# Performance work log

Measured on AMD Instinct MI355X. Metric: run time of the kernel, lower is better.

Reference implementation:

```python
import jax, jax.numpy as jnp
import numpy as np

K_HOP = 2

def _graph_conv(x, A, W, b):
    feats = [x]
    xk = x
    for _ in range(K_HOP):
        xk = jnp.einsum('bmn,bnc->bmc', A, xk)
        feats.append(xk)
    return jnp.concatenate(feats, -1) @ W + b

def _pair_mlp(y, W2, b2, W1, b1, shape):
    # normal_conv: fc1(relu(fc2(y))).reshape(shape)
    return (jax.nn.relu(y @ W2 + b2) @ W1 + b1).reshape(shape)

def setup_inputs():
    key = jax.random.key(0)
    ks = jax.random.split(key, 16)
    B, T, N = 8, 12, 200
    C_IN, H, D, H_ST = 2, 64, 32, 64
    def lin(k, fi, fo):
        k1, k2 = jax.random.split(k)
        s = 1.0 / float(np.sqrt(fi))
        return (jax.random.uniform(k1, (fi, fo), jnp.float32, -s, s),
                jax.random.uniform(k2, (fo,), jnp.float32, -s, s))
    W_s2d, b_s2d = lin(ks[0], H_ST, D)
    W_rz, b_rz = lin(ks[1], 1 + D, 2 * D)
    W_h, b_h = lin(ks[2], 1 + D, D)
    Wc2, bc2 = lin(ks[3], 2 * D, D)
    Wc1, bc1 = lin(ks[4], D, 1)
    Wm2, bm2 = lin(ks[5], 2 * D, D)
    Wm1, bm1 = lin(ks[6], D, 1)
    gin = (C_IN + H) * (1 + K_HOP)
    W_ru, b_ru = lin(ks[7], gin, 2 * H)
    W_cand, b_cand = lin(ks[8], gin, H)
    Wp1, bp1 = lin(ks[9], H, H)
    Wp2, bp2 = lin(ks[10], H, 1)
    x = jax.random.normal(ks[11], (B, T, N, C_IN), jnp.float32)
    node_fea_st = jax.random.normal(ks[12], (N, H_ST), jnp.float32)
    return dict(x=x, node_fea_st=node_fea_st, W_s2d=W_s2d, b_s2d=b_s2d,
                W_rz=W_rz, b_rz=b_rz, W_h=W_h, b_h=b_h,
                Wc2=Wc2, bc2=bc2, Wc1=Wc1, bc1=bc1,
                Wm2=Wm2, bm2=bm2, Wm1=Wm1, bm1=bm1,
                W_ru=W_ru, b_ru=b_ru, W_cand=W_cand, b_cand=b_cand,
                Wp1=Wp1, bp1=bp1, Wp2=Wp2, bp2=bp2)

def reference(x, node_fea_st, W_s2d, b_s2d, W_rz, b_rz, W_h, b_h,
              Wc2, bc2, Wc1, bc1, Wm2, bm2, Wm1, bm1,
              W_ru, b_ru, W_cand, b_cand, Wp1, bp1, Wp2, bp2):
    B, T, N, _ = x.shape
    H = W_cand.shape[1]
    D = W_h.shape[1]
    # states_dy init: linear_s2d(node_fea_st) broadcast over batch
    state_dy0 = jnp.broadcast_to((node_fea_st @ W_s2d + b_s2d)[None], (B, N, D))
    state0 = jnp.zeros((B, N, H), x.dtype)
    xs = jnp.transpose(x, (1, 0, 2, 3))  # [T,B,N,C]

    def step(carry, xt):
        state, state_dy = carry
        inp1 = xt[..., :1]
        # DynamicGraphGRU (conv_method='normal')
        rz = jax.nn.sigmoid(jnp.concatenate([inp1, state_dy], -1) @ W_rz + b_rz)
        r, z = jnp.split(rz, 2, -1)
        h = jnp.tanh(jnp.concatenate([inp1, r * state_dy], -1) @ W_h + b_h)
        new_dy = z * state_dy + (1.0 - z) * h
        s = jax.nn.relu(new_dy)  # [B,N,D]
        y = jnp.concatenate([jnp.broadcast_to(s[:, :, None, :], (B, N, N, D)),
                             jnp.broadcast_to(s[:, None, :, :], (B, N, N, D))], -1)
        g = _pair_mlp(y, Wc2, bc2, Wc1, bc1, (B, N, N))
        m = _pair_mlp(y, Wm2, bm2, Wm1, bm1, (B, N, N))
        A = g * jax.nn.sigmoid(m)  # dynamic graph [B,N,N]
        # DCGRUCell with supports=[A]
        ru = jax.nn.sigmoid(_graph_conv(jnp.concatenate([xt, state], -1), A, W_ru, b_ru))
        rr, u = jnp.split(ru, 2, -1)
        c = jnp.tanh(_graph_conv(jnp.concatenate([xt, rr * state], -1), A, W_cand, b_cand))
        new_state = u * state + (1.0 - u) * c
        return (new_state, new_dy), A

    (state, _), dy_graphs = jax.lax.scan(step, (state0, state_dy0), xs)
    # predictor: Linear -> LeakyReLU -> Linear
    pred = jax.nn.leaky_relu(state @ Wp1 + bp1) @ Wp2 + bp2  # [B,N,1]
    return pred, dy_graphs
```

## Files before the change

kernel.cpp:

```cpp
#include <hip/hip_runtime.h>
#include <math.h>

#define B_ 8
#define T_ 12
#define N_ 200
#define R_ 1600
#define NN_ 40000

__device__ __forceinline__ float sigm(float v) { return 1.f / (1.f + expf(-v)); }

__global__ void __launch_bounds__(256) k_dyall(
        const float* __restrict__ x,  const float* __restrict__ nf,
        const float* __restrict__ Ws2d, const float* __restrict__ bs2d,
        const float* __restrict__ Wrz,  const float* __restrict__ brz,
        const float* __restrict__ Wh,   const float* __restrict__ bh,
        const float* __restrict__ Wc2,  const float* __restrict__ Wm2,
        const float* __restrict__ bc2,  const float* __restrict__ bm2,
        float* __restrict__ Pc, float* __restrict__ Qc,
        float* __restrict__ Pm, float* __restrict__ Qm,
        float* __restrict__ state) {
    __shared__ alignas(16) float sWs2d[64 * 32];
    __shared__ alignas(16) float sWrzT[64][36];
    __shared__ alignas(16) float sWhT[32][36];
    __shared__ alignas(16) float sWc2T[32][68];
    __shared__ alignas(16) float sWm2T[32][68];
    __shared__ float sbrz[64], sbh[32], sbs2d[32], sbc2[32], sbm2[32];
    __shared__ alignas(16) float nfs[4][64], dy[4][32], rz[4][64], s4[4][32];
    __shared__ alignas(16) float in1[4][36], in2[4][36];
    int bk = blockIdx.x, tid = threadIdx.x;
    int w = tid >> 6, o = tid & 63;
    int row = bk * 4 + w, b = row / N_, n = row % N_;
    state[bk * 256 + tid] = 0.f;
    for (int idx = tid; idx < 2048; idx += 256) sWs2d[idx] = Ws2d[idx];
    for (int idx = tid; idx < 2304; idx += 256) {
        int oo = idx / 36, ii = idx % 36;
        sWrzT[oo][ii] = (ii < 33) ? Wrz[ii * 64 + oo] : 0.f;
    }
    for (int idx = tid; idx < 1152; idx += 256) {
        int kk = idx / 36, ii = idx % 36;
        sWhT[kk][ii] = (ii < 33) ? Wh[ii * 32 + kk] : 0.f;
    }
    for (int idx = tid; idx < 2176; idx += 256) {
        int kk = idx / 68, rr = idx % 68;
        float vc = (rr < 64) ? Wc2[rr * 32 + kk] : 0.f;
        float vm = (rr < 64) ? Wm2[rr * 32 + kk] : 0.f;
        sWc2T[kk][rr] = vc; sWm2T[kk][rr] = vm;
    }
    if (tid < 144) { ((float*)in1)[tid] = 0.f; ((float*)in2)[tid] = 0.f; }
    if (tid < 64) sbrz[tid] = brz[tid];
    if (tid < 32) { sbh[tid] = bh[tid]; sbs2d[tid] = bs2d[tid];
                    sbc2[tid] = bc2[tid]; sbm2[tid] = bm2[tid]; }
    nfs[w][o] = nf[n * 64 + o];
    __syncthreads();
    if (o < 32) {
        float acc = sbs2d[o];
        #pragma unroll 8
        for (int i = 0; i < 64; ++i) acc += nfs[w][i] * sWs2d[i * 32 + o];
        dy[w][o] = acc;
    }
    __syncthreads();
    for (int t = 0; t < T_; ++t) {
        if (o == 0) { float v = x[((b * T_ + t) * N_ + n) * 2]; in1[w][0] = v; in2[w][0] = v; }
        if (o < 32) in1[w][o + 1] = dy[w][o];
        __syncthreads();
        float acc = sbrz[o];
        #pragma unroll
        for (int ig = 0; ig < 9; ++ig) {
            float4 w4 = *(const float4*)&sWrzT[o][4 * ig];
            float4 f4 = *(const float4*)&in1[w][4 * ig];
            acc += f4.x * w4.x + f4.y * w4.y + f4.z * w4.z + f4.w * w4.w;
        }
        rz[w][o] = sigm(acc);
        __syncthreads();
        if (o < 32) in2[w][o + 1] = rz[w][o] * dy[w][o];
        __syncthreads();
        if (o < 32) {
            float h = sbh[o];
            #pragma unroll
            for (int ig = 0; ig < 9; ++ig) {
                float4 w4 = *(const float4*)&sWhT[o][4 * ig];
                float4 f4 = *(const float4*)&in2[w][4 * ig];
                h += f4.x * w4.x + f4.y * w4.y + f4.z * w4.z + f4.w * w4.w;
            }
            h = tanhf(h);
            float z = rz[w][32 + o];
            float nd = z * dy[w][o] + (1.f - z) * h;
            dy[w][o] = nd;
            s4[w][o] = nd > 0.f ? nd : 0.f;
        }
        __syncthreads();
        size_t base = ((size_t)t * R_ + row) * 32;
        for (int idx = o; idx < 128; idx += 64) {
            int mat = idx >> 5, k = idx & 31;
            const float* WT = (mat < 2) ? &sWc2T[k][0] : &sWm2T[k][0];
            int rb = (mat & 1) ? 32 : 0;
            float a = (mat == 0) ? sbc2[k] : (mat == 2) ? sbm2[k] : 0.f;
            #pragma unroll
            for (int ig = 0; ig < 8; ++ig) {
                float4 w4 = *(const float4*)&WT[rb + 4 * ig];
                float4 f4 = *(const float4*)&s4[w][4 * ig];
                a += f4.x * w4.x + f4.y * w4.y + f4.z * w4.z + f4.w * w4.w;
            }
            ((mat == 0) ? Pc : (mat == 1) ? Qc : (mat == 2) ? Pm : Qm)[base + k] = a;
        }
        __syncthreads();
    }
}

__global__ void __launch_bounds__(256) k_pairall(
        const float* __restrict__ Pc, const float* __restrict__ Qc,
        const float* __restrict__ Pm, const float* __restrict__ Qm,
        const float* __restrict__ Wc1, const float* __restrict__ bc1,
        const float* __restrict__ Wm1, const float* __restrict__ bm1,
        float* __restrict__ out) {
    __shared__ float sPc[16][36], sQc[16][36], sPm[16][36], sQm[16][36];
    int z = blockIdx.z;
    int i0 = blockIdx.x * 16, j0 = blockIdx.y * 16;
    int tid = threadIdx.y * 16 + threadIdx.x;
    size_t tb = (size_t)z * N_;
    for (int l = tid; l < 128; l += 256) {
        int r = l >> 3, q = l & 7;
        int gi = i0 + r, gj = j0 + r;
        float4 z4 = make_float4(0.f, 0.f, 0.f, 0.f);
        *(float4*)&sPc[r][4 * q] = (gi < N_) ? *(const float4*)&Pc[(tb + gi) * 32 + 4 * q] : z4;
        *(float4*)&sPm[r][4 * q] = (gi < N_) ? *(const float4*)&Pm[(tb + gi) * 32 + 4 * q] : z4;
        *(float4*)&sQc[r][4 * q] = (gj < N_) ? *(const float4*)&Qc[(tb + gj) * 32 + 4 * q] : z4;
        *(float4*)&sQm[r][4 * q] = (gj < N_) ? *(const float4*)&Qm[(tb + gj) * 32 + 4 * q] : z4;
    }
    float4 wc[8], wm[8];
    #pragma unroll
    for (int kg = 0; kg < 8; ++kg) {
        wc[kg] = *(const float4*)&Wc1[4 * kg];
        wm[kg] = *(const float4*)&Wm1[4 * kg];
    }
    __syncthreads();
    int i = i0 + threadIdx.y, j = j0 + threadIdx.x;
    if (i >= N_ || j >= N_) return;
    int ty = threadIdx.y, tx = threadIdx.x;
    float g0 = 0.f, g1 = 0.f, m0 = 0.f, m1 = 0.f;
    #pragma unroll
    for (int kg = 0; kg < 8; ++kg) {
        float4 pc = *(const float4*)&sPc[ty][4 * kg];
        float4 qc = *(const float4*)&sQc[tx][4 * kg];
        float4 w4 = wc[kg];
        g0 += fmaxf(pc.x + qc.x, 0.f) * w4.x + fmaxf(pc.y + qc.y, 0.f) * w4.y;
        g1 += fmaxf(pc.z + qc.z, 0.f) * w4.z + fmaxf(pc.w + qc.w, 0.f) * w4.w;
        float4 pm = *(const float4*)&sPm[ty][4 * kg];
        float4 qm = *(const float4*)&sQm[tx][4 * kg];
        float4 v4 = wm[kg];
        m0 += fmaxf(pm.x + qm.x, 0.f) * v4.x + fmaxf(pm.y + qm.y, 0.f) * v4.y;
        m1 += fmaxf(pm.z + qm.z, 0.f) * v4.z + fmaxf(pm.w + qm.w, 0.f) * v4.w;
    }
    float g = g0 + g1 + bc1[0];
    float m = m0 + m1 + bm1[0];
    out[R_ + (((size_t)z * N_ + i) * N_ + j)] = g * sigm(m);
}

__global__ void __launch_bounds__(256) k_a2(
        const float* __restrict__ Abase, float* __restrict__ Cbase, int nmat) {
    __shared__ float Ast[32][132];
    __shared__ float Bs[32][68];
    int bx = blockIdx.x;
    int z = bx % nmat, tl = bx / nmat;
    int i0 = (tl >> 2) * 128, j0 = (tl & 3) * 64;
    const float* Az = Abase + (size_t)z * NN_;
    float* Cz = Cbase + (size_t)z * NN_;
    int tid = threadIdx.x;
    int tx = tid & 15, ty = tid >> 4;
    float acc[8][4] = {};
    for (int k0 = 0; k0 < 200; k0 += 32) {
        {
            int i = tid >> 1;
            int kb = (tid & 1) * 16;
            int gi = i0 + i;
            #pragma unroll
            for (int q = 0; q < 4; ++q) {
                int k = kb + q * 4;
                int gk = k0 + k;
                float4 v = make_float4(0.f, 0.f, 0.f, 0.f);
                if (gi < N_) {
                    if (gk + 3 < N_) v = *(const float4*)&Az[gi * N_ + gk];
                    else {
                        float t0 = (gk + 0 < N_) ? Az[gi * N_ + gk + 0] : 0.f;
                        float t1 = (gk + 1 < N_) ? Az[gi * N_ + gk + 1] : 0.f;
                        float t2 = (gk + 2 < N_) ? Az[gi * N_ + gk + 2] : 0.f;
                        float t3 = (gk + 3 < N_) ? Az[gi * N_ + gk + 3] : 0.f;
                        v = make_float4(t0, t1, t2, t3);
                    }
                }
                Ast[k + 0][i] = v.x; Ast[k + 1][i] = v.y;
                Ast[k + 2][i] = v.z; Ast[k + 3][i] = v.w;
            }
        }
        {
            #pragma unroll
            for (int q = 0; q < 2; ++q) {
                int id = tid + 256 * q;
                int k = id >> 4, jq = (id & 15) * 4;
                int gk = k0 + k, gj = j0 + jq;
                float4 v = make_float4(0.f, 0.f, 0.f, 0.f);
                if (gk < N_) {
                    if (gj + 3 < N_) v = *(const float4*)&Az[gk * N_ + gj];
                    else {
                        float t0 = (gj + 0 < N_) ? Az[gk * N_ + gj + 0] : 0.f;
                        float t1 = (gj + 1 < N_) ? Az[gk * N_ + gj + 1] : 0.f;
                        float t2 = (gj + 2 < N_) ? Az[gk * N_ + gj + 2] : 0.f;
                        float t3 = (gj + 3 < N_) ? Az[gk * N_ + gj + 3] : 0.f;
                        v = make_float4(t0, t1, t2, t3);
                    }
                }
                *(float4*)&Bs[k][jq] = v;
            }
        }
        __syncthreads();
        #pragma unroll 8
        for (int k = 0; k < 32; ++k) {
            float4 a0 = *(const float4*)&Ast[k][ty * 8];
            float4 a1 = *(const float4*)&Ast[k][ty * 8 + 4];
            float4 bv = *(const float4*)&Bs[k][tx * 4];
            acc[0][0] += a0.x * bv.x; acc[0][1] += a0.x * bv.y; acc[0][2] += a0.x * bv.z; acc[0][3] += a0.x * bv.w;
            acc[1][0] += a0.y * bv.x; acc[1][1] += a0.y * bv.y; acc[1][2] += a0.y * bv.z; acc[1][3] += a0.y * bv.w;
            acc[2][0] += a0.z * bv.x; acc[2][1] += a0.z * bv.y; acc[2][2] += a0.z * bv.z; acc[2][3] += a0.z * bv.w;
            acc[3][0] += a0.w * bv.x; acc[3][1] += a0.w * bv.y; acc[3][2] += a0.w * bv.z; acc[3][3] += a0.w * bv.w;
            acc[4][0] += a1.x * bv.x; acc[4][1] += a1.x * bv.y; acc[4][2] += a1.x * bv.z; acc[4][3] += a1.x * bv.w;
            acc[5][0] += a1.y * bv.x; acc[5][1] += a1.y * bv.y; acc[5][2] += a1.y * bv.z; acc[5][3] += a1.y * bv.w;
            acc[6][0] += a1.z * bv.x; acc[6][1] += a1.z * bv.y; acc[6][2] += a1.z * bv.z; acc[6][3] += a1.z * bv.w;
            acc[7][0] += a1.w * bv.x; acc[7][1] += a1.w * bv.y; acc[7][2] += a1.w * bv.z; acc[7][3] += a1.w * bv.w;
        }
        __syncthreads();
    }
    #pragma unroll
    for (int r = 0; r < 8; ++r) {
        int gi = i0 + ty * 8 + r;
        if (gi >= N_) continue;
        int gj = j0 + tx * 4;
        if (gj + 3 < N_) {
            *(float4*)&Cz[gi * N_ + gj] = make_float4(acc[r][0], acc[r][1], acc[r][2], acc[r][3]);
        } else {
            #pragma unroll
            for (int e = 0; e < 4; ++e) if (gj + e < N_) Cz[gi * N_ + gj + e] = acc[r][e];
        }
    }
}

__global__ void __launch_bounds__(256) k_xh(
        const float* __restrict__ Abase, const float* __restrict__ A2base,
        const float* __restrict__ x, int z0, float* __restrict__ xh) {
    __shared__ float xtl[400];
    int zl = blockIdx.x, tid = threadIdx.x;
    int z = z0 + zl, t = z >> 3, b = z & 7;
    int w = tid >> 6, l = tid & 63;
    const float* xb = x + ((size_t)(b * T_ + t)) * N_ * 2;
    for (int idx = tid; idx < 400; idx += 256) xtl[idx] = xb[idx];
    __syncthreads();
    for (int it = 0; it < 50; ++it) {
        int i = it * 4 + w;
        float p0 = 0.f, p1 = 0.f, p2 = 0.f, p3 = 0.f;
        if (l < 50) {
            float4 a4 = *(const float4*)(Abase + (size_t)zl * NN_ + i * 200 + 4 * l);
            float4 c4 = *(const float4*)(A2base + (size_t)zl * NN_ + i * 200 + 4 * l);
            #pragma unroll
            for (int q = 0; q < 4; ++q) {
                float av = (&a4.x)[q], cv = (&c4.x)[q];
                float x0 = xtl[(4 * l + q) * 2], x1 = xtl[(4 * l + q) * 2 + 1];
                p0 += av * x0; p1 += av * x1; p2 += cv * x0; p3 += cv * x1;
            }
        }
        #pragma unroll
        for (int off = 32; off > 0; off >>= 1) {
            p0 += __shfl_down(p0, off); p1 += __shfl_down(p1, off);
            p2 += __shfl_down(p2, off); p3 += __shfl_down(p3, off);
        }
        if (l == 0) *(float4*)(xh + ((size_t)zl * N_ + i) * 4) = make_float4(p0, p1, p2, p3);
    }
}

__global__ void __launch_bounds__(256) k_ru2(
        const float* __restrict__ At, const float* __restrict__ A2t,
        const float* __restrict__ xht,
        const float* __restrict__ x, int t, const float* __restrict__ state,
        const float* __restrict__ Wru, const float* __restrict__ bru,
        float* __restrict__ rs, float* __restrict__ ub) {
    __shared__ float a2s[2 * 200], c2s[2 * 200];
    __shared__ float hpA[4][64], hpC[4][64];
    __shared__ float feat[2][200];
    __shared__ float gp[8][2][128];
    int bx = blockIdx.x;
    int b = bx & 7, i0 = (bx >> 3) * 2;
    int tid = threadIdx.x;
    const float* F = state + (size_t)b * (N_ * 64);
    {
        const float4* Ar = (const float4*)(At + ((size_t)b * N_ + i0) * 200);
        const float4* Cr = (const float4*)(A2t + ((size_t)b * N_ + i0) * 200);
        if (tid < 100) { ((float4*)a2s)[tid] = Ar[tid]; ((float4*)c2s)[tid] = Cr[tid]; }
        if (tid >= 100 && tid < 164) {
            int l = tid - 100, r = l >> 5, q = l & 31;
            *(float2*)&feat[r][2 + 2 * q] = *(const float2*)&F[(size_t)(i0 + r) * 64 + 2 * q];
        }
        if (tid >= 164 && tid < 168) {
            int l = tid - 164;
            feat[l >> 1][l & 1] = x[((size_t)(b * T_ + t) * N_ + i0 + (l >> 1)) * 2 + (l & 1)];
        }
        if (tid >= 168 && tid < 176) {
            int l = tid - 168, rr = l >> 2, q = l & 3;
            feat[rr][(q < 2) ? (66 + q) : (132 + q - 2)] = xht[((size_t)b * N_ + i0 + rr) * 4 + q];
        }
    }
    __syncthreads();
    {
        int w = tid >> 6, lane = tid & 63;
        int r = w & 1, h = w >> 1;
        int cg = lane & 15, jq = lane >> 4;
        const float* ar = a2s + r * 200 + h * 100;
        const float* cr = c2s + r * 200 + h * 100;
        const float* Fb = F + (size_t)(h * 100) * 64 + 4 * cg;
        float4 accA = make_float4(0.f, 0.f, 0.f, 0.f);
        float4 accC = make_float4(0.f, 0.f, 0.f, 0.f);
        #pragma unroll 5
        for (int m = 0; m < 25; ++m) {
            int j = jq + 4 * m;
            float av = ar[j], cv = cr[j];
            float4 f4 = *(const float4*)&Fb[(size_t)j * 64];
            accA.x += av * f4.x; accA.y += av * f4.y; accA.z += av * f4.z; accA.w += av * f4.w;
            accC.x += cv * f4.x; accC.y += cv * f4.y; accC.z += cv * f4.z; accC.w += cv * f4.w;
        }
        accA.x += __shfl_xor(accA.x, 16); accA.y += __shfl_xor(accA.y, 16);
        accA.z += __shfl_xor(accA.z, 16); accA.w += __shfl_xor(accA.w, 16);
        accC.x += __shfl_xor(accC.x, 16); accC.y += __shfl_xor(accC.y, 16);
        accC.z += __shfl_xor(accC.z, 16); accC.w += __shfl_xor(accC.w, 16);
        accA.x += __shfl_xor(accA.x, 32); accA.y += __shfl_xor(accA.y, 32);
        accA.z += __shfl_xor(accA.z, 32); accA.w += __shfl_xor(accA.w, 32);
        accC.x += __shfl_xor(accC.x, 32); accC.y += __shfl_xor(accC.y, 32);
        accC.z += __shfl_xor(accC.z, 32); accC.w += __shfl_xor(accC.w, 32);
        if (lane < 16) {
            *(float4*)&hpA[w][4 * cg] = accA;
            *(float4*)&hpC[w][4 * cg] = accC;
        }
    }
    __syncthreads();
    {
        int mt = tid >> 7, r = (tid >> 6) & 1, c = tid & 63;
        float v = mt ? (hpC[r][c] + hpC[2 + r][c]) : (hpA[r][c] + hpA[2 + r][c]);
        feat[r][(mt ? 134 : 68) + c] = v;
    }
    __syncthreads();
    {
        int cq = tid & 31, kh = tid >> 5;
        int k0 = 25 * kh, kend = (k0 + 25 < 198) ? (k0 + 25) : 198;
        float4 s0 = make_float4(0.f, 0.f, 0.f, 0.f);
        float4 s1 = make_float4(0.f, 0.f, 0.f, 0.f);
        for (int k = k0; k < kend; ++k) {
            float4 w4 = *(const float4*)&Wru[(size_t)k * 128 + 4 * cq];
            float f0 = feat[0][k], f1 = feat[1][k];
            s0.x += f0 * w4.x; s0.y += f0 * w4.y; s0.z += f0 * w4.z; s0.w += f0 * w4.w;
            s1.x += f1 * w4.x; s1.y += f1 * w4.y; s1.z += f1 * w4.z; s1.w += f1 * w4.w;
        }
        *(float4*)&gp[kh][0][4 * cq] = s0;
        *(float4*)&gp[kh][1][4 * cq] = s1;
    }
    __syncthreads();
    {
        int rq = tid >> 7, c = tid & 127;
        float a = bru[c];
        #pragma unroll
        for (int h = 0; h < 8; ++h) a += gp[h][rq][c];
        float v = sigm(a);
        size_t go = (size_t)b * N_ + i0 + rq;
        if (c < 64) rs[go * 64 + c] = v * feat[rq][2 + c];
        else        ub[go * 64 + (c - 64)] = v;
    }
}

__global__ void __launch_bounds__(256) k_cand2(
        const float* __restrict__ At, const float* __restrict__ A2t,
        const float* __restrict__ xht,
        const float* __restrict__ x, int t, const float* __restrict__ rsin,
        const float* __restrict__ Wcd, const float* __restrict__ bcd,
        const float* __restrict__ ub, float* __restrict__ state) {
    __shared__ float a2s[2 * 200], c2s[2 * 200];
    __shared__ float hpA[4][64], hpC[4][64];
    __shared__ float feat[2][200];
    __shared__ float gp[16][2][64];
    int bx = blockIdx.x;
    int b = bx & 7, i0 = (bx >> 3) * 2;
    int tid = threadIdx.x;
    const float* F = rsin + (size_t)b * (N_ * 64);
    {
        const float4* Ar = (const float4*)(At + ((size_t)b * N_ + i0) * 200);
        const float4* Cr = (const float4*)(A2t + ((size_t)b * N_ + i0) * 200);
        if (tid < 100) { ((float4*)a2s)[tid] = Ar[tid]; ((float4*)c2s)[tid] = Cr[tid]; }
        if (tid >= 100 && tid < 164) {
            int l = tid - 100, r = l >> 5, q = l & 31;
            *(float2*)&feat[r][2 + 2 * q] = *(const float2*)&F[(size_t)(i0 + r) * 64 + 2 * q];
        }
        if (tid >= 164 && tid < 168) {
            int l = tid - 164;
            feat[l >> 1][l & 1] = x[((size_t)(b * T_ + t) * N_ + i0 + (l >> 1)) * 2 + (l & 1)];
        }
        if (tid >= 168 && tid < 176) {
            int l = tid - 168, rr = l >> 2, q = l & 3;
            feat[rr][(q < 2) ? (66 + q) : (132 + q - 2)] = xht[((size_t)b * N_ + i0 + rr) * 4 + q];
        }
    }
    __syncthreads();
    {
        int w = tid >> 6, lane = tid & 63;
        int r = w & 1, h = w >> 1;
        int cg = lane & 15, jq = lane >> 4;
        const float* ar = a2s + r * 200 + h * 100;
        const float* cr = c2s + r * 200 + h * 100;
        const float* Fb = F + (size_t)(h * 100) * 64 + 4 * cg;
        float4 accA = make_float4(0.f, 0.f, 0.f, 0.f);
        float4 accC = make_float4(0.f, 0.f, 0.f, 0.f);
        #pragma unroll 5
        for (int m = 0; m < 25; ++m) {
            int j = jq + 4 * m;
            float av = ar[j], cv = cr[j];
            float4 f4 = *(const float4*)&Fb[(size_t)j * 64];
            accA.x += av * f4.x; accA.y += av * f4.y; accA.z += av * f4.z; accA.w += av * f4.w;
            accC.x += cv * f4.x; accC.y += cv * f4.y; accC.z += cv * f4.z; accC.w += cv * f4.w;
        }
        accA.x += __shfl_xor(accA.x, 16); accA.y += __shfl_xor(accA.y, 16);
        accA.z += __shfl_xor(accA.z, 16); accA.w += __shfl_xor(accA.w, 16);
        accC.x += __shfl_xor(accC.x, 16); accC.y += __shfl_xor(accC.y, 16);
        accC.z += __shfl_xor(accC.z, 16); accC.w += __shfl_xor(accC.w, 16);
        accA.x += __shfl_xor(accA.x, 32); accA.y += __shfl_xor(accA.y, 32);
        accA.z += __shfl_xor(accA.z, 32); accA.w += __shfl_xor(accA.w, 32);
        accC.x += __shfl_xor(accC.x, 32); accC.y += __shfl_xor(accC.y, 32);
        accC.z += __shfl_xor(accC.z, 32); accC.w += __shfl_xor(accC.w, 32);
        if (lane < 16) {
            *(float4*)&hpA[w][4 * cg] = accA;
            *(float4*)&hpC[w][4 * cg] = accC;
        }
    }
    __syncthreads();
    {
        int mt = tid >> 7, r = (tid >> 6) & 1, c = tid & 63;
        float v = mt ? (hpC[r][c] + hpC[2 + r][c]) : (hpA[r][c] + hpA[2 + r][c]);
        feat[r][(mt ? 134 : 68) + c] = v;
    }
    __syncthreads();
    {
        int cq = tid & 15, kh = tid >> 4;
        int k0 = 13 * kh, kend = (k0 + 13 < 198) ? (k0 + 13) : 198;
        float4 s0 = make_float4(0.f, 0.f, 0.f, 0.f);
        float4 s1 = make_float4(0.f, 0.f, 0.f, 0.f);
        for (int k = k0; k < kend; ++k) {
            float4 w4 = *(const float4*)&Wcd[(size_t)k * 64 + 4 * cq];
            float f0 = feat[0][k], f1 = feat[1][k];
            s0.x += f0 * w4.x; s0.y += f0 * w4.y; s0.z += f0 * w4.z; s0.w += f0 * w4.w;
            s1.x += f1 * w4.x; s1.y += f1 * w4.y; s1.z += f1 * w4.z; s1.w += f1 * w4.w;
        }
        *(float4*)&gp[kh][0][4 * cq] = s0;
        *(float4*)&gp[kh][1][4 * cq] = s1;
    }
    __syncthreads();
    if (tid < 128) {
        int rq = tid >> 6, c = tid & 63;
        float a = bcd[c];
        #pragma unroll
        for (int h = 0; h < 16; ++h) a += gp[h][rq][c];
        size_t go = (size_t)b * N_ + i0 + rq;
        float cnd = tanhf(a);
        float u = ub[go * 64 + c];
        float st = state[go * 64 + c];
        state[go * 64 + c] = u * st + (1.f - u) * cnd;
    }
}

__global__ void __launch_bounds__(64) k_pred(
        const float* __restrict__ state,
        const float* __restrict__ Wp1, const float* __restrict__ bp1,
        const float* __restrict__ Wp2, const float* __restrict__ bp2,
        float* __restrict__ out) {
    __shared__ float st[64];
    int row = blockIdx.x;
    int tid = threadIdx.x;
    st[tid] = state[row * 64 + tid];
    __syncthreads();
    float acc = bp1[tid];
    #pragma unroll 8
    for (int a = 0; a < 64; ++a) acc += st[a] * Wp1[a * 64 + tid];
    acc = acc > 0.f ? acc : 0.01f * acc;
    float v = acc * Wp2[tid];
    #pragma unroll
    for (int off = 32; off > 0; off >>= 1) v += __shfl_down(v, off);
    if (tid == 0) out[row] = v + bp2[0];
}

extern "C" void kernel_launch(void* const* d_in, const int* in_sizes, int n_in,
                              void* d_out, int out_size, void* d_ws, size_t ws_size,
                              hipStream_t stream) {
    const float* x    = (const float*)d_in[0];
    const float* nf   = (const float*)d_in[1];
    const float* Ws2d = (const float*)d_in[2];
    const float* bs2d = (const float*)d_in[3];
    const float* Wrz  = (const float*)d_in[4];
    const float* brz  = (const float*)d_in[5];
    const float* Wh   = (const float*)d_in[6];
    const float* bh   = (const float*)d_in[7];
    const float* Wc2  = (const float*)d_in[8];
    const float* bc2  = (const float*)d_in[9];
    const float* Wc1  = (const float*)d_in[10];
    const float* bc1  = (const float*)d_in[11];
    const float* Wm2  = (const float*)d_in[12];
    const float* bm2  = (const float*)d_in[13];
    const float* Wm1  = (const float*)d_in[14];
    const float* bm1  = (const float*)d_in[15];
    const float* Wru  = (const float*)d_in[16];
    const float* bru  = (const float*)d_in[17];
    const float* Wcand= (const float*)d_in[18];
    const float* bcand= (const float*)d_in[19];
    const float* Wp1  = (const float*)d_in[20];
    const float* bp1  = (const float*)d_in[21];
    const float* Wp2  = (const float*)d_in[22];
    const float* bp2  = (const float*)d_in[23];
    float* out = (float*)d_out;

    float* ws = (float*)d_ws;
    const size_t PQ = (size_t)T_ * R_ * 32;
    float* Pc = ws;
    float* Qc = Pc + PQ;
    float* Pm = Qc + PQ;
    float* Qm = Pm + PQ;

    const size_t A2F = (size_t)96 * NN_;
    const size_t XHF = (size_t)96 * N_ * 4;
    const size_t FULL_NEED = (A2F + XHF + 3 * (size_t)R_ * 64) * 4;
    bool full = ws_size >= FULL_NEED;

    const float* Aall = out + R_;

    if (full) {
        float* A2base = ws;
        float* xhbase = ws + A2F;
        float* state  = xhbase + XHF;
        float* rs     = state + (size_t)R_ * 64;
        float* ub     = rs + (size_t)R_ * 64;

        k_dyall<<<400, 256, 0, stream>>>(x, nf, Ws2d, bs2d, Wrz, brz, Wh, bh,
                                         Wc2, Wm2, bc2, bm2, Pc, Qc, Pm, Qm, state);
        k_pairall<<<dim3(13, 13, 96), dim3(16, 16), 0, stream>>>(
            Pc, Qc, Pm, Qm, Wc1, bc1, Wm1, bm1, out);
        k_a2<<<96 * 8, 256, 0, stream>>>(Aall, A2base, 96);
        k_xh<<<96, 256, 0, stream>>>(Aall, A2base, x, 0, xhbase);

        for (int t = 0; t < T_; ++t) {
            const float* At  = Aall + (size_t)t * 8 * NN_;
            const float* A2t = A2base + (size_t)t * 8 * NN_;
            const float* xht = xhbase + (size_t)t * 8 * N_ * 4;
            k_ru2  <<<800, 256, 0, stream>>>(At, A2t, xht, x, t, state, Wru, bru, rs, ub);
            k_cand2<<<800, 256, 0, stream>>>(At, A2t, xht, x, t, rs, Wcand, bcand, ub, state);
        }
        k_pred<<<R_, 64, 0, stream>>>(state, Wp1, bp1, Wp2, bp2, out);
    } else {
        float* A2base = ws + 4 * PQ;
        float* xhbase = A2base + (size_t)8 * NN_;
        float* state  = xhbase + (size_t)8 * N_ * 4;
        float* rs     = state + (size_t)R_ * 64;
        float* ub     = rs + (size_t)R_ * 64;

        k_dyall<<<400, 256, 0, stream>>>(x, nf, Ws2d, bs2d, Wrz, brz, Wh, bh,
                                         Wc2, Wm2, bc2, bm2, Pc, Qc, Pm, Qm, state);
        k_pairall<<<dim3(13, 13, 96), dim3(16, 16), 0, stream>>>(
            Pc, Qc, Pm, Qm, Wc1, bc1, Wm1, bm1, out);
        for (int t = 0; t < T_; ++t) {
            const float* At = Aall + (size_t)t * 8 * NN_;
            k_a2<<<8 * 8, 256, 0, stream>>>(At, A2base, 8);
            k_xh<<<8, 256, 0, stream>>>(At, A2base, x, t * 8, xhbase);
            k_ru2  <<<800, 256, 0, stream>>>(At, A2base, xhbase, x, t, state, Wru, bru, rs, ub);
            k_cand2<<<800, 256, 0, stream>>>(At, A2base, xhbase, x, t, rs, Wcand, bcand, ub, state);
        }
        k_pred<<<R_, 64, 0, stream>>>(state, Wp1, bp1, Wp2, bp2, out);
    }
}
```

Baseline: 469.5 us.

## Overlap graph aggregation with partial linear projection via warp specialization

In k_ru2 and k_cand2, the first two warps now do the A·F and A²·F aggregation for both rows at once, sharing each F load. Meanwhile the other two warps compute the linear-layer partial sums over the first 68 feature columns, which are already known. The remaining 130 columns are projected after the aggregated features are written. This hides part of the projection behind the aggregation at the cost of an extra barrier and half the threads doing aggregation.

```diff
diff --git a/kernel.cpp b/kernel.cpp
--- a/kernel.cpp
+++ b/kernel.cpp
@@ -282,9 +282,9 @@
         const float* __restrict__ Wru, const float* __restrict__ bru,
         float* __restrict__ rs, float* __restrict__ ub) {
     __shared__ float a2s[2 * 200], c2s[2 * 200];
-    __shared__ float hpA[4][64], hpC[4][64];
+    __shared__ float hpA[2][2][64], hpC[2][2][64];
     __shared__ float feat[2][200];
-    __shared__ float gp[8][2][128];
+    __shared__ float gp[12][2][128];
     int bx = blockIdx.x;
     int b = bx & 7, i0 = (bx >> 3) * 2;
     int tid = threadIdx.x;
@@ -307,46 +307,47 @@
         }
     }
     __syncthreads();
-    {
-        int w = tid >> 6, lane = tid & 63;
-        int r = w & 1, h = w >> 1;
+    int w = tid >> 6, lane = tid & 63;
+    if (w < 2) {
+        int h = w;
         int cg = lane & 15, jq = lane >> 4;
-        const float* ar = a2s + r * 200 + h * 100;
-        const float* cr = c2s + r * 200 + h * 100;
+        const float* a0p = a2s + h * 100;
+        const float* a1p = a2s + 200 + h * 100;
+        const float* c0p = c2s + h * 100;
+        const float* c1p = c2s + 200 + h * 100;
         const float* Fb = F + (size_t)(h * 100) * 64 + 4 * cg;
-        float4 accA = make_float4(0.f, 0.f, 0.f, 0.f);
-        float4 accC = make_float4(0.f, 0.f, 0.f, 0.f);
+        float4 aA0 = make_float4(0.f, 0.f, 0.f, 0.f), aA1 = aA0, aC0 = aA0, aC1 = aA0;
         #pragma unroll 5
         for (int m = 0; m < 25; ++m) {
             int j = jq + 4 * m;
-            float av = ar[j], cv = cr[j];
             float4 f4 = *(const float4*)&Fb[(size_t)j * 64];
-            accA.x += av * f4.x; accA.y += av * f4.y; accA.z += av * f4.z; accA.w += av * f4.w;
-            accC.x += cv * f4.x; accC.y += cv * f4.y; accC.z += cv * f4.z; accC.w += cv * f4.w;
-        }
-        accA.x += __shfl_xor(accA.x, 16); accA.y += __shfl_xor(accA.y, 16);
-        accA.z += __shfl_xor(accA.z, 16); accA.w += __shfl_xor(accA.w, 16);
-        accC.x += __shfl_xor(accC.x, 16); accC.y += __shfl_xor(accC.y, 16);
-        accC.z += __shfl_xor(accC.z, 16); accC.w += __shfl_xor(accC.w, 16);
-        accA.x += __shfl_xor(accA.x, 32); accA.y += __shfl_xor(accA.y, 32);
-        accA.z += __shfl_xor(accA.z, 32); accA.w += __shfl_xor(accA.w, 32);
-        accC.x += __shfl_xor(accC.x, 32); accC.y += __shfl_xor(accC.y, 32);
-        accC.z += __shfl_xor(accC.z, 32); accC.w += __shfl_xor(accC.w, 32);
+            float a0 = a0p[j], a1 = a1p[j], c0 = c0p[j], c1 = c1p[j];
+            aA0.x += a0 * f4.x; aA0.y += a0 * f4.y; aA0.z += a0 * f4.z; aA0.w += a0 * f4.w;
+            aA1.x += a1 * f4.x; aA1.y += a1 * f4.y; aA1.z += a1 * f4.z; aA1.w += a1 * f4.w;
+            aC0.x += c0 * f4.x; aC0.y += c0 * f4.y; aC0.z += c0 * f4.z; aC0.w += c0 * f4.w;
+            aC1.x += c1 * f4.x; aC1.y += c1 * f4.y; aC1.z += c1 * f4.z; aC1.w += c1 * f4.w;
+        }
+        #pragma unroll
+        for (int off = 16; off <= 32; off <<= 1) {
+            aA0.x += __shfl_xor(aA0.x, off); aA0.y += __shfl_xor(aA0.y, off);
+            aA0.z += __shfl_xor(aA0.z, off); aA0.w += __shfl_xor(aA0.w, off);
+            aA1.x += __shfl_xor(aA1.x, off); aA1.y += __shfl_xor(aA1.y, off);
+            aA1.z += __shfl_xor(aA1.z, off); aA1.w += __shfl_xor(aA1.w, off);
+            aC0.x += __shfl_xor(aC0.x, off); aC0.y += __shfl_xor(aC0.y, off);
+            aC0.z += __shfl_xor(aC0.z, off); aC0.w += __shfl_xor(aC0.w, off);
+            aC1.x += __shfl_xor(aC1.x, off); aC1.y += __shfl_xor(aC1.y, off);
+            aC1.z += __shfl_xor(aC1.z, off); aC1.w += __shfl_xor(aC1.w, off);
+        }
         if (lane < 16) {
-            *(float4*)&hpA[w][4 * cg] = accA;
-            *(float4*)&hpC[w][4 * cg] = accC;
-        }
-    }
-    __syncthreads();
-    {
-        int mt = tid >> 7, r = (tid >> 6) & 1, c = tid & 63;
-        float v = mt ? (hpC[r][c] + hpC[2 + r][c]) : (hpA[r][c] + hpA[2 + r][c]);
-        feat[r][(mt ? 134 : 68) + c] = v;
-    }
-    __syncthreads();
-    {
-        int cq = tid & 31, kh = tid >> 5;
-        int k0 = 25 * kh, kend = (k0 + 25 < 198) ? (k0 + 25) : 198;
+            *(float4*)&hpA[h][0][4 * cg] = aA0;
+            *(float4*)&hpA[h][1][4 * cg] = aA1;
+            *(float4*)&hpC[h][0][4 * cg] = aC0;
+            *(float4*)&hpC[h][1][4 * cg] = aC1;
+        }
+    } else {
+        int l = tid - 128;
+        int cq = l & 31, kh = l >> 5;
+        int k0 = 17 * kh, kend = (k0 + 17 < 68) ? (k0 + 17) : 68;
         float4 s0 = make_float4(0.f, 0.f, 0.f, 0.f);
         float4 s1 = make_float4(0.f, 0.f, 0.f, 0.f);
         for (int k = k0; k < kend; ++k) {
@@ -360,10 +361,31 @@
     }
     __syncthreads();
     {
+        int mt = tid >> 7, r = (tid >> 6) & 1, c = tid & 63;
+        float v = mt ? (hpC[0][r][c] + hpC[1][r][c]) : (hpA[0][r][c] + hpA[1][r][c]);
+        feat[r][(mt ? 134 : 68) + c] = v;
+    }
+    __syncthreads();
+    {
+        int cq = tid & 31, kh = tid >> 5;
+        int k0 = 68 + 17 * kh, kend = (k0 + 17 < 198) ? (k0 + 17) : 198;
+        float4 s0 = make_float4(0.f, 0.f, 0.f, 0.f);
+        float4 s1 = make_float4(0.f, 0.f, 0.f, 0.f);
+        for (int k = k0; k < kend; ++k) {
+            float4 w4 = *(const float4*)&Wru[(size_t)k * 128 + 4 * cq];
+            float f0 = feat[0][k], f1 = feat[1][k];
+            s0.x += f0 * w4.x; s0.y += f0 * w4.y; s0.z += f0 * w4.z; s0.w += f0 * w4.w;
+            s1.x += f1 * w4.x; s1.y += f1 * w4.y; s1.z += f1 * w4.z; s1.w += f1 * w4.w;
+        }
+        *(float4*)&gp[4 + kh][0][4 * cq] = s0;
+        *(float4*)&gp[4 + kh][1][4 * cq] = s1;
+    }
+    __syncthreads();
+    {
         int rq = tid >> 7, c = tid & 127;
         float a = bru[c];
         #pragma unroll
-        for (int h = 0; h < 8; ++h) a += gp[h][rq][c];
+        for (int h = 0; h < 12; ++h) a += gp[h][rq][c];
         float v = sigm(a);
         size_t go = (size_t)b * N_ + i0 + rq;
         if (c < 64) rs[go * 64 + c] = v * feat[rq][2 + c];
@@ -378,9 +400,9 @@
         const float* __restrict__ Wcd, const float* __restrict__ bcd,
         const float* __restrict__ ub, float* __restrict__ state) {
     __shared__ float a2s[2 * 200], c2s[2 * 200];
-    __shared__ float hpA[4][64], hpC[4][64];
+    __shared__ float hpA[2][2][64], hpC[2][2][64];
     __shared__ float feat[2][200];
-    __shared__ float gp[16][2][64];
+    __shared__ float gp[24][2][64];
     int bx = blockIdx.x;
     int b = bx & 7, i0 = (bx >> 3) * 2;
     int tid = threadIdx.x;
@@ -403,46 +425,47 @@
         }
     }
     __syncthreads();
-    {
-        int w = tid >> 6, lane = tid & 63;
-        int r = w & 1, h = w >> 1;
+    int w = tid >> 6, lane = tid & 63;
+    if (w < 2) {
+        int h = w;
         int cg = lane & 15, jq = lane >> 4;
-        const float* ar = a2s + r * 200 + h * 100;
-        const float* cr = c2s + r * 200 + h * 100;
+        const float* a0p = a2s + h * 100;
+        const float* a1p = a2s + 200 + h * 100;
+        const float* c0p = c2s + h * 100;
+        const float* c1p = c2s + 200 + h * 100;
         const float* Fb = F + (size_t)(h * 100) * 64 + 4 * cg;
-        float4 accA = make_float4(0.f, 0.f, 0.f, 0.f);
-        float4 accC = make_float4(0.f, 0.f, 0.f, 0.f);
+        float4 aA0 = make_float4(0.f, 0.f, 0.f, 0.f), aA1 = aA0, aC0 = aA0, aC1 = aA0;
         #pragma unroll 5
         for (int m = 0; m < 25; ++m) {
             int j = jq + 4 * m;
-            float av = ar[j], cv = cr[j];
             float4 f4 = *(const float4*)&Fb[(size_t)j * 64];
-            accA.x += av * f4.x; accA.y += av * f4.y; accA.z += av * f4.z; accA.w += av * f4.w;
-            accC.x += cv * f4.x; accC.y += cv * f4.y; accC.z += cv * f4.z; accC.w += cv * f4.w;
-        }
-        accA.x += __shfl_xor(accA.x, 16); accA.y += __shfl_xor(accA.y, 16);
-        accA.z += __shfl_xor(accA.z, 16); accA.w += __shfl_xor(accA.w, 16);
-        accC.x += __shfl_xor(accC.x, 16); accC.y += __shfl_xor(accC.y, 16);
-        accC.z += __shfl_xor(accC.z, 16); accC.w += __shfl_xor(accC.w, 16);
-        accA.x += __shfl_xor(accA.x, 32); accA.y += __shfl_xor(accA.y, 32);
-        accA.z += __shfl_xor(accA.z, 32); accA.w += __shfl_xor(accA.w, 32);
-        accC.x += __shfl_xor(accC.x, 32); accC.y += __shfl_xor(accC.y, 32);
-        accC.z += __shfl_xor(accC.z, 32); accC.w += __shfl_xor(accC.w, 32);
+            float a0 = a0p[j], a1 = a1p[j], c0 = c0p[j], c1 = c1p[j];
+            aA0.x += a0 * f4.x; aA0.y += a0 * f4.y; aA0.z += a0 * f4.z; aA0.w += a0 * f4.w;
+            aA1.x += a1 * f4.x; aA1.y += a1 * f4.y; aA1.z += a1 * f4.z; aA1.w += a1 * f4.w;
+            aC0.x += c0 * f4.x; aC0.y += c0 * f4.y; aC0.z += c0 * f4.z; aC0.w += c0 * f4.w;
+            aC1.x += c1 * f4.x; aC1.y += c1 * f4.y; aC1.z += c1 * f4.z; aC1.w += c1 * f4.w;
+        }
+        #pragma unroll
+        for (int off = 16; off <= 32; off <<= 1) {
+            aA0.x += __shfl_xor(aA0.x, off); aA0.y += __shfl_xor(aA0.y, off);
+            aA0.z += __shfl_xor(aA0.z, off); aA0.w += __shfl_xor(aA0.w, off);
+            aA1.x += __shfl_xor(aA1.x, off); aA1.y += __shfl_xor(aA1.y, off);
+            aA1.z += __shfl_xor(aA1.z, off); aA1.w += __shfl_xor(aA1.w, off);
+            aC0.x += __shfl_xor(aC0.x, off); aC0.y += __shfl_xor(aC0.y, off);
+            aC0.z += __shfl_xor(aC0.z, off); aC0.w += __shfl_xor(aC0.w, off);
+            aC1.x += __shfl_xor(aC1.x, off); aC1.y += __shfl_xor(aC1.y, off);
+            aC1.z += __shfl_xor(aC1.z, off); aC1.w += __shfl_xor(aC1.w, off);
+        }
         if (lane < 16) {
-            *(float4*)&hpA[w][4 * cg] = accA;
-            *(float4*)&hpC[w][4 * cg] = accC;
-        }
-    }
-    __syncthreads();
-    {
-        int mt = tid >> 7, r = (tid >> 6) & 1, c = tid & 63;
-        float v = mt ? (hpC[r][c] + hpC[2 + r][c]) : (hpA[r][c] + hpA[2 + r][c]);
-        feat[r][(mt ? 134 : 68) + c] = v;
-    }
-    __syncthreads();
-    {
-        int cq = tid & 15, kh = tid >> 4;
-        int k0 = 13 * kh, kend = (k0 + 13 < 198) ? (k0 + 13) : 198;
+            *(float4*)&hpA[h][0][4 * cg] = aA0;
+            *(float4*)&hpA[h][1][4 * cg] = aA1;
+            *(float4*)&hpC[h][0][4 * cg] = aC0;
+            *(float4*)&hpC[h][1][4 * cg] = aC1;
+        }
+    } else {
+        int l = tid - 128;
+        int cq = l & 15, kh = l >> 4;
+        int k0 = 9 * kh, kend = (k0 + 9 < 68) ? (k0 + 9) : 68;
         float4 s0 = make_float4(0.f, 0.f, 0.f, 0.f);
         float4 s1 = make_float4(0.f, 0.f, 0.f, 0.f);
         for (int k = k0; k < kend; ++k) {
@@ -455,11 +478,33 @@
         *(float4*)&gp[kh][1][4 * cq] = s1;
     }
     __syncthreads();
+    {
+        int mt = tid >> 7, r = (tid >> 6) & 1, c = tid & 63;
+        float v = mt ? (hpC[0][r][c] + hpC[1][r][c]) : (hpA[0][r][c] + hpA[1][r][c]);
+        feat[r][(mt ? 134 : 68) + c] = v;
+    }
+    __syncthreads();
+    {
+        int cq = tid & 15, kh = tid >> 4;
+        int k0 = 68 + 9 * kh;
+        int kend = (k0 + 9 < 198) ? (k0 + 9) : 198;
+        float4 s0 = make_float4(0.f, 0.f, 0.f, 0.f);
+        float4 s1 = make_float4(0.f, 0.f, 0.f, 0.f);
+        for (int k = k0; k < kend; ++k) {
+            float4 w4 = *(const float4*)&Wcd[(size_t)k * 64 + 4 * cq];
+            float f0 = feat[0][k], f1 = feat[1][k];
+            s0.x += f0 * w4.x; s0.y += f0 * w4.y; s0.z += f0 * w4.z; s0.w += f0 * w4.w;
+            s1.x += f1 * w4.x; s1.y += f1 * w4.y; s1.z += f1 * w4.z; s1.w += f1 * w4.w;
+        }
+        *(float4*)&gp[8 + kh][0][4 * cq] = s0;
+        *(float4*)&gp[8 + kh][1][4 * cq] = s1;
+    }
+    __syncthreads();
     if (tid < 128) {
         int rq = tid >> 6, c = tid & 63;
         float a = bcd[c];
         #pragma unroll
-        for (int h = 0; h < 16; ++h) a += gp[h][rq][c];
+        for (int h = 0; h < 24; ++h) a += gp[h][rq][c];
         size_t go = (size_t)b * N_ + i0 + rq;
         float cnd = tanhf(a);
         float u = ub[go * 64 + c];
```

After: 452.5 us (median of 2 runs). 1.04x faster.
